# Kernel optimization log

Measured on AMD Instinct MI355X. Metric: run time of the kernel, lower is better.

## Reference

```python
import jax, jax.numpy as jnp
import numpy as np

B, N = 256, 64          # molecules, atoms per molecule
EMB = 64                # atom embedding dim
G = 64                  # n_gaussians
HID = 128               # interaction hidden
OUT = 512               # output_dim
GAUSS_WIDTH = 0.5


def setup_inputs() -> dict:
    key = jax.random.key(0)
    ks = jax.random.split(key, 10)
    atomic_nums = jax.random.randint(ks[0], (B, N), 0, 120, dtype=jnp.int64 if jax.config.x64_enabled else jnp.int32)
    coords = jax.random.normal(ks[1], (B, N, 3), dtype=jnp.float32) * 3.0
    embed_table = jax.random.normal(ks[2], (120, EMB), dtype=jnp.float32)
    # interaction: Linear(128->128), GELU, Linear(128->128); weights stored (in, out)
    W1 = jax.random.normal(ks[3], (EMB + G, HID), dtype=jnp.float32) / np.sqrt(EMB + G)
    b1 = jnp.zeros((HID,), dtype=jnp.float32)
    W2 = jax.random.normal(ks[4], (HID, HID), dtype=jnp.float32) / np.sqrt(HID)
    b2 = jnp.zeros((HID,), dtype=jnp.float32)
    # output_proj: Linear(128 -> 512)
    Wo = jax.random.normal(ks[5], (HID, OUT), dtype=jnp.float32) / np.sqrt(HID)
    bo = jnp.zeros((OUT,), dtype=jnp.float32)
    centers = jnp.linspace(0.0, 10.0, G).astype(jnp.float32)
    return {"atomic_nums": atomic_nums, "coords": coords, "embed_table": embed_table,
            "W1": W1, "b1": b1, "W2": W2, "b2": b2, "Wo": Wo, "bo": bo, "centers": centers}


def reference(atomic_nums, coords, embed_table, W1, b1, W2, b2, Wo, bo, centers):
    # per-atom embedding: [B,N,EMB]
    emb = embed_table[atomic_nums]
    # pairwise distances: [B,N,N]; guard sqrt(0) for diagonal
    diff = coords[:, :, None, :] - coords[:, None, :, :]
    sq = jnp.sum(diff * diff, axis=-1)
    pos = sq > 0
    dists = jnp.where(pos, jnp.sqrt(jnp.where(pos, sq, 1.0)), 0.0)
    # Gaussian smearing: [B,N,N,G]
    gauss = jnp.exp(-0.5 * jnp.square((dists[..., None] - centers) / GAUSS_WIDTH))
    # mean over neighbor axis j: [B,N,G]
    avg_gauss = gauss.mean(axis=2)
    feat = jnp.concatenate([emb, avg_gauss], axis=-1)  # [B,N,EMB+G]
    h = jax.nn.gelu(feat @ W1 + b1, approximate=False) @ W2 + b2  # [B,N,HID]
    mol = h.mean(axis=1)  # [B,HID]
    return mol @ Wo + bo  # [B,OUT]
```

## Files before the change

### kernel.cpp

```cpp
#include <hip/hip_runtime.h>
#include <math.h>

namespace {
constexpr int NB   = 256;
constexpr int NA   = 64;
constexpr int EMBD = 64;
constexpr int HIDD = 128;
constexpr int OUTD = 512;
constexpr int FPS  = 136;
constexpr int DSTR = 68;

typedef __attribute__((ext_vector_type(8))) short bfrag8;
typedef __attribute__((ext_vector_type(4))) float floatx4;

__device__ __forceinline__ unsigned short bf16_rne(float f) {
    unsigned u = __float_as_uint(f);
    u += 0x7fffu + ((u >> 16) & 1u);
    return (unsigned short)(u >> 16);
}

__device__ __forceinline__ float gelu_fast(float x) {
    const float ax = fabsf(x) * 0.7071067811865475f;
    const float t  = __builtin_amdgcn_rcpf(fmaf(0.3275911f, ax, 1.0f));
    float p = fmaf(1.061405429f, t, -1.453152027f);
    p = fmaf(p, t, 1.421413741f);
    p = fmaf(p, t, -0.284496736f);
    p = fmaf(p, t, 0.254829592f);
    p = p * t;
    const float e = __builtin_amdgcn_exp2f(-1.4426950408889634f * ax * ax);
    const float erfx = copysignf(fmaf(-p, e, 1.0f), x);
    const float hx   = 0.5f * x;
    return fmaf(hx, erfx, hx);
}


__global__ __launch_bounds__(1024, 1)
void mlip_fused(const int*   __restrict__ atomic_nums,
                const float* __restrict__ coords,
                const float* __restrict__ embed_table,
                const float* __restrict__ W1, const float* __restrict__ b1,
                const float* __restrict__ W2, const float* __restrict__ b2,
                const float* __restrict__ Wo, const float* __restrict__ bo,
                const float* __restrict__ centers,
                float*       __restrict__ out)
{
    const int b    = blockIdx.x;
    const int tid  = threadIdx.x;
    const int lane = tid & 63;
    const int wid  = tid >> 6;

    __shared__ float s_dist[NA * DSTR];
    __shared__ short s_w[16384];
    __shared__ short s_fhi[NA][FPS];
    __shared__ float s_molS[HIDD];
    __shared__ float s_molv[HIDD];

    const int wn      = wid >> 2;
    const int lrow    = lane & 15, g4 = lane >> 4;
    const int arow    = ((wid & 3) << 4) + lrow;
    const int colbase = (wn << 5) + lrow;

    const int gcol = tid & 127, kc = tid >> 7;
    const int colT = tid >> 1, kh = tid & 1;

    const int grow = tid >> 4;
    const int gch  = (tid >> 2) & 3;
    const int jq   = tid & 3;

    const float bo_r = bo[colT];
    const float b1a  = b1[colbase];
    const float b1b  = b1[colbase + 16];
    const float b2r  = b2[gcol];
    const float c0   = centers[gch << 4];

    if (tid < HIDD) s_molS[tid] = 0.0f;

    float w1v[16];
#pragma unroll
    for (int a = 0; a < 2; ++a) {
        const int slot = (a << 10) + tid;
        const int fg = slot >> 6, ls = slot & 63;
        const int k0 = ((fg >> 3) << 5) + ((ls >> 4) << 3);
        const int n  = ((fg & 7) << 4) + (ls & 15);
        const float* src = W1 + (size_t)k0 * HIDD + n;
#pragma unroll
        for (int r = 0; r < 8; ++r) w1v[a * 8 + r] = src[(size_t)r * HIDD];
    }

    const float* cbase = coords + (size_t)b * NA * 3;
    const float cx = cbase[lane * 3 + 0];
    const float cy = cbase[lane * 3 + 1];
    const float cz = cbase[lane * 3 + 2];
    {
        const int i = tid >> 4, e4 = (tid & 15) << 2;
        const int z = atomic_nums[b * NA + i];
        const float4 ev = *(const float4*)(embed_table + (size_t)z * EMBD + e4);
        short4 h4;
        const float v[4] = {ev.x, ev.y, ev.z, ev.w};
        short* hp = (short*)&h4;
#pragma unroll
        for (int q = 0; q < 4; ++q) hp[q] = (short)bf16_rne(v[q]);
        *(short4*)&s_fhi[i][e4] = h4;
    }

#pragma unroll
    for (int it = 0; it < 4; ++it) {
        const int i = (wid << 2) + it;
        const float xi = __shfl(cx, i, 64);
        const float yi = __shfl(cy, i, 64);
        const float zi = __shfl(cz, i, 64);
        const float dx = xi - cx, dy = yi - cy, dz = zi - cz;
        const float sq = dx * dx + dy * dy + dz * dz;
        s_dist[i * DSTR + lane] = sq > 0.0f ? sqrtf(sq) : 0.0f;
    }

#pragma unroll
    for (int a = 0; a < 2; ++a) {
        unsigned Hu[4];
#pragma unroll
        for (int p = 0; p < 4; ++p) {
            const float x = w1v[a * 8 + 2 * p], y = w1v[a * 8 + 2 * p + 1];
            unsigned h;
            asm("v_cvt_pk_bf16_f32 %0, %1, %2" : "=v"(h) : "v"(x), "v"(y));
            Hu[p] = h;
        }
        const int slot = (a << 10) + tid;
        const int base = ((slot >> 6) << 9) + (slot & 63) * 8;
        *(uint4*)&s_w[base] = make_uint4(Hu[0], Hu[1], Hu[2], Hu[3]);
    }

    {
        constexpr float L2E   = 1.4426950408889634f;
        constexpr float DELTA = 10.0f / 63.0f;
        constexpr float K2L   = -2.0f * L2E;
        constexpr float UA    = 4.0f * DELTA * L2E;
        const float P1  = 0.95085835f,  P2  = 0.81745274f, P3  = 0.63539088f,
                    P4  = 0.44653019f,  P5  = 0.28372112f, P6  = 0.16299117f,
                    P7  = 0.08465801f,  P8  = 0.03975530f, P9  = 0.01688004f,
                    P10 = 0.00647989f,  P11 = 0.00224901f, P12 = 0.00070576f,
                    P13 = 0.00020024f,  P14 = 5.136543e-5f, P15 = 1.191313e-5f;

        float acc[16];
#pragma unroll
        for (int q = 0; q < 16; ++q) acc[q] = 0.0f;

        const float* drow = &s_dist[grow * DSTR + (jq << 4)];
#pragma unroll
        for (int j4 = 0; j4 < 4; ++j4) {
            const float4 d4 = *(const float4*)(drow + (j4 << 2));
            const float dv[4] = {d4.x, d4.y, d4.z, d4.w};
#pragma unroll
            for (int jj = 0; jj < 4; ++jj) {
                const float x  = dv[jj] - c0;
                const float A  = __builtin_amdgcn_exp2f(K2L * x * x);
                const float r  = __builtin_amdgcn_exp2f(UA * x);
                const float r2 = r * r, r4 = r2 * r2;
                float s0 = A, s1 = A * r, s2 = A * r2, s3 = s1 * r2;
                acc[0] += s0;
                acc[1]  = fmaf(s1, P1,  acc[1]);
                acc[2]  = fmaf(s2, P2,  acc[2]);
                acc[3]  = fmaf(s3, P3,  acc[3]);
                s0 *= r4; s1 *= r4; s2 *= r4; s3 *= r4;
                acc[4]  = fmaf(s0, P4,  acc[4]);
                acc[5]  = fmaf(s1, P5,  acc[5]);
                acc[6]  = fmaf(s2, P6,  acc[6]);
                acc[7]  = fmaf(s3, P7,  acc[7]);
                s0 *= r4; s1 *= r4; s2 *= r4; s3 *= r4;
                acc[8]  = fmaf(s0, P8,  acc[8]);
                acc[9]  = fmaf(s1, P9,  acc[9]);
                acc[10] = fmaf(s2, P10, acc[10]);
                acc[11] = fmaf(s3, P11, acc[11]);
                s0 *= r4; s1 *= r4; s2 *= r4; s3 *= r4;
                acc[12] = fmaf(s0, P12, acc[12]);
                acc[13] = fmaf(s1, P13, acc[13]);
                acc[14] = fmaf(s2, P14, acc[14]);
                acc[15] = fmaf(s3, P15, acc[15]);
            }
        }
#pragma unroll
        for (int q = 0; q < 16; ++q) {
            acc[q] += __shfl_xor(acc[q], 1, 64);
            acc[q] += __shfl_xor(acc[q], 2, 64);
        }
        if (jq == 0) {
            unsigned* hp = (unsigned*)&s_fhi[grow][EMBD + (gch << 4)];
#pragma unroll
            for (int q2 = 0; q2 < 8; ++q2) {
                const unsigned h0 = bf16_rne(acc[2 * q2]     * (1.0f / 64.0f));
                const unsigned h1 = bf16_rne(acc[2 * q2 + 1] * (1.0f / 64.0f));
                hp[q2] = h0 | (h1 << 16);
            }
        }
    }
    __syncthreads();

    float wo_a[32];
    float w2r[16];
    {
        floatx4 acc0 = {0,0,0,0}, acc1 = {0,0,0,0};
#pragma unroll
        for (int ks = 0; ks < 4; ++ks) {
            const int k0 = (ks << 5) + (g4 << 3);
            const bfrag8 ahi = *(const bfrag8*)&s_fhi[arow][k0];
#pragma unroll
            for (int nt = 0; nt < 2; ++nt) {
                const int base = ((((ks << 3) + (wn << 1) + nt) << 6) + lane) << 3;
                const bfrag8 bhi = *(const bfrag8*)&s_w[base];
                if (nt) acc1 = __builtin_amdgcn_mfma_f32_16x16x32_bf16(ahi, bhi, acc1, 0, 0, 0);
                else    acc0 = __builtin_amdgcn_mfma_f32_16x16x32_bf16(ahi, bhi, acc0, 0, 0, 0);
            }
        }

        {
            const float* wop = Wo + ((size_t)(kh << 6)) * OUTD + colT;
#pragma unroll
            for (int k = 0; k < 32; ++k) wo_a[k] = wop[(size_t)k * OUTD];
            const float* src = W2 + (size_t)(kc << 4) * HIDD + gcol;
#pragma unroll
            for (int q = 0; q < 16; ++q) w2r[q] = src[(size_t)q * HIDD];
        }

#pragma unroll
        for (int nt = 0; nt < 2; ++nt) {
            const float bb = nt ? b1b : b1a;
            const floatx4 a = nt ? acc1 : acc0;
            float s = gelu_fast(a[0] + bb) + gelu_fast(a[1] + bb)
                    + gelu_fast(a[2] + bb) + gelu_fast(a[3] + bb);
            s += __shfl_xor(s, 16, 64);
            s += __shfl_xor(s, 32, 64);
            if (lane < 16) atomicAdd(&s_molS[colbase + (nt << 4)], s);
        }
    }
    __syncthreads();

    float wo_b[32];
    {
        float acc = 0.0f;
        const int kb = kc << 4;
        float4 m4[4];
#pragma unroll
        for (int p = 0; p < 4; ++p) m4[p] = *(const float4*)&s_molS[kb + (p << 2)];
        const float* ms = (const float*)m4;
#pragma unroll
        for (int q = 0; q < 16; ++q) acc = fmaf(ms[q], w2r[q], acc);
        s_dist[(kc << 7) + gcol] = acc;

        const float* wop = Wo + ((size_t)((kh << 6) + 32)) * OUTD + colT;
#pragma unroll
        for (int k = 0; k < 32; ++k) wo_b[k] = wop[(size_t)k * OUTD];
    }
    __syncthreads();

    if (tid < HIDD) {
        float m = 0.0f;
#pragma unroll
        for (int p = 0; p < 8; ++p) m += s_dist[(p << 7) + tid];
        s_molv[tid] = m * (1.0f / 64.0f) + b2r;
    }
    __syncthreads();

    {
        const float* mp = &s_molv[kh << 6];
        float a = 0.0f;
#pragma unroll
        for (int k = 0; k < 32; ++k) a = fmaf(mp[k], wo_a[k], a);
#pragma unroll
        for (int k = 0; k < 32; ++k) a = fmaf(mp[32 + k], wo_b[k], a);
        a += __shfl_xor(a, 1, 64);
        if (kh == 0)
            out[(size_t)b * OUTD + colT] = a + bo_r;
    }
}
}

extern "C" void kernel_launch(void* const* d_in, const int* in_sizes, int n_in,
                              void* d_out, int out_size, void* d_ws, size_t ws_size,
                              hipStream_t stream) {
    const int*   atomic_nums = (const int*)  d_in[0];
    const float* coords      = (const float*)d_in[1];
    const float* embed_table = (const float*)d_in[2];
    const float* W1          = (const float*)d_in[3];
    const float* b1          = (const float*)d_in[4];
    const float* W2          = (const float*)d_in[5];
    const float* b2          = (const float*)d_in[6];
    const float* Wo          = (const float*)d_in[7];
    const float* bo          = (const float*)d_in[8];
    const float* centers     = (const float*)d_in[9];
    float*       out         = (float*)d_out;

    mlip_fused<<<NB, 1024, 0, stream>>>(atomic_nums, coords, embed_table,
                                        W1, b1, W2, b2, Wo, bo, centers, out);
}
```

Measured before the change: 21.65 us.

## Split fused kernel into per-half-molecule front kernel and separate output projection tail

The single 1024-thread-per-molecule kernel becomes two kernels. The front kernel uses 512 threads per half molecule (512 blocks) to compute features, the W1 MFMA, GELU and the W2 reduction, then writes partial per-molecule vectors to workspace. A second tail kernel sums the two halves, adds b2 and applies the Wo projection. The aim is better occupancy, with fewer registers and less LDS per block and no Wo preloading in registers. The cost is a second launch, a workspace round trip, and each block still staging the full W1 into LDS.

```diff
diff --git a/kernel.cpp b/kernel.cpp
--- a/kernel.cpp
+++ b/kernel.cpp
@@ -33,52 +33,47 @@
     return fmaf(hx, erfx, hx);
 }
 
-
-__global__ __launch_bounds__(1024, 1)
-void mlip_fused(const int*   __restrict__ atomic_nums,
+__global__ __launch_bounds__(512, 4)
+void mlip_front(const int*   __restrict__ atomic_nums,
                 const float* __restrict__ coords,
                 const float* __restrict__ embed_table,
                 const float* __restrict__ W1, const float* __restrict__ b1,
-                const float* __restrict__ W2, const float* __restrict__ b2,
-                const float* __restrict__ Wo, const float* __restrict__ bo,
+                const float* __restrict__ W2,
                 const float* __restrict__ centers,
-                float*       __restrict__ out)
+                float*       __restrict__ ws)
 {
-    const int b    = blockIdx.x;
+    const int bid  = blockIdx.x;
+    const int mol  = bid >> 1, h = bid & 1;
     const int tid  = threadIdx.x;
     const int lane = tid & 63;
     const int wid  = tid >> 6;
 
-    __shared__ float s_dist[NA * DSTR];
+    __shared__ float s_dist[32 * DSTR];
     __shared__ short s_w[16384];
-    __shared__ short s_fhi[NA][FPS];
+    __shared__ short s_fhi[32][FPS];
     __shared__ float s_molS[HIDD];
-    __shared__ float s_molv[HIDD];
-
-    const int wn      = wid >> 2;
+
+    const int wn      = wid >> 1;
     const int lrow    = lane & 15, g4 = lane >> 4;
-    const int arow    = ((wid & 3) << 4) + lrow;
+    const int arow    = ((wid & 1) << 4) + lrow;
     const int colbase = (wn << 5) + lrow;
 
     const int gcol = tid & 127, kc = tid >> 7;
-    const int colT = tid >> 1, kh = tid & 1;
 
     const int grow = tid >> 4;
     const int gch  = (tid >> 2) & 3;
     const int jq   = tid & 3;
 
-    const float bo_r = bo[colT];
-    const float b1a  = b1[colbase];
-    const float b1b  = b1[colbase + 16];
-    const float b2r  = b2[gcol];
-    const float c0   = centers[gch << 4];
+    const float b1a = b1[colbase];
+    const float b1b = b1[colbase + 16];
+    const float c0  = centers[gch << 4];
 
     if (tid < HIDD) s_molS[tid] = 0.0f;
 
     float w1v[16];
 #pragma unroll
     for (int a = 0; a < 2; ++a) {
-        const int slot = (a << 10) + tid;
+        const int slot = (a << 9) + tid;
         const int fg = slot >> 6, ls = slot & 63;
         const int k0 = ((fg >> 3) << 5) + ((ls >> 4) << 3);
         const int n  = ((fg & 7) << 4) + (ls & 15);
@@ -87,13 +82,14 @@
         for (int r = 0; r < 8; ++r) w1v[a * 8 + r] = src[(size_t)r * HIDD];
     }
 
-    const float* cbase = coords + (size_t)b * NA * 3;
+    const float* cbase = coords + (size_t)mol * NA * 3;
     const float cx = cbase[lane * 3 + 0];
     const float cy = cbase[lane * 3 + 1];
     const float cz = cbase[lane * 3 + 2];
+
     {
         const int i = tid >> 4, e4 = (tid & 15) << 2;
-        const int z = atomic_nums[b * NA + i];
+        const int z = atomic_nums[mol * NA + (h << 5) + i];
         const float4 ev = *(const float4*)(embed_table + (size_t)z * EMBD + e4);
         short4 h4;
         const float v[4] = {ev.x, ev.y, ev.z, ev.w};
@@ -105,10 +101,11 @@
 
 #pragma unroll
     for (int it = 0; it < 4; ++it) {
-        const int i = (wid << 2) + it;
-        const float xi = __shfl(cx, i, 64);
-        const float yi = __shfl(cy, i, 64);
-        const float zi = __shfl(cz, i, 64);
+        const int i  = (wid << 2) + it;
+        const int gi = (h << 5) + i;
+        const float xi = __shfl(cx, gi, 64);
+        const float yi = __shfl(cy, gi, 64);
+        const float zi = __shfl(cz, gi, 64);
         const float dx = xi - cx, dy = yi - cy, dz = zi - cz;
         const float sq = dx * dx + dy * dy + dz * dz;
         s_dist[i * DSTR + lane] = sq > 0.0f ? sqrtf(sq) : 0.0f;
@@ -120,13 +117,24 @@
 #pragma unroll
         for (int p = 0; p < 4; ++p) {
             const float x = w1v[a * 8 + 2 * p], y = w1v[a * 8 + 2 * p + 1];
-            unsigned h;
-            asm("v_cvt_pk_bf16_f32 %0, %1, %2" : "=v"(h) : "v"(x), "v"(y));
-            Hu[p] = h;
-        }
-        const int slot = (a << 10) + tid;
+            unsigned hh;
+            asm("v_cvt_pk_bf16_f32 %0, %1, %2" : "=v"(hh) : "v"(x), "v"(y));
+            Hu[p] = hh;
+        }
+        const int slot = (a << 9) + tid;
         const int base = ((slot >> 6) << 9) + (slot & 63) * 8;
         *(uint4*)&s_w[base] = make_uint4(Hu[0], Hu[1], Hu[2], Hu[3]);
+    }
+
+#pragma unroll
+    for (int a = 0; a < 2; ++a) {
+        const int slot = ((a + 2) << 9) + tid;
+        const int fg = slot >> 6, ls = slot & 63;
+        const int k0 = ((fg >> 3) << 5) + ((ls >> 4) << 3);
+        const int n  = ((fg & 7) << 4) + (ls & 15);
+        const float* src = W1 + (size_t)k0 * HIDD + n;
+#pragma unroll
+        for (int r = 0; r < 8; ++r) w1v[a * 8 + r] = src[(size_t)r * HIDD];
     }
 
     {
@@ -192,10 +200,24 @@
             }
         }
     }
+
+#pragma unroll
+    for (int a = 0; a < 2; ++a) {
+        unsigned Hu[4];
+#pragma unroll
+        for (int p = 0; p < 4; ++p) {
+            const float x = w1v[a * 8 + 2 * p], y = w1v[a * 8 + 2 * p + 1];
+            unsigned hh;
+            asm("v_cvt_pk_bf16_f32 %0, %1, %2" : "=v"(hh) : "v"(x), "v"(y));
+            Hu[p] = hh;
+        }
+        const int slot = ((a + 2) << 9) + tid;
+        const int base = ((slot >> 6) << 9) + (slot & 63) * 8;
+        *(uint4*)&s_w[base] = make_uint4(Hu[0], Hu[1], Hu[2], Hu[3]);
+    }
     __syncthreads();
 
-    float wo_a[32];
-    float w2r[16];
+    float w2ra[16];
     {
         floatx4 acc0 = {0,0,0,0}, acc1 = {0,0,0,0};
 #pragma unroll
@@ -212,12 +234,9 @@
         }
 
         {
-            const float* wop = Wo + ((size_t)(kh << 6)) * OUTD + colT;
-#pragma unroll
-            for (int k = 0; k < 32; ++k) wo_a[k] = wop[(size_t)k * OUTD];
-            const float* src = W2 + (size_t)(kc << 4) * HIDD + gcol;
-#pragma unroll
-            for (int q = 0; q < 16; ++q) w2r[q] = src[(size_t)q * HIDD];
+            const float* src = W2 + (size_t)(kc << 5) * HIDD + gcol;
+#pragma unroll
+            for (int q = 0; q < 16; ++q) w2ra[q] = src[(size_t)q * HIDD];
         }
 
 #pragma unroll
@@ -233,43 +252,57 @@
     }
     __syncthreads();
 
-    float wo_b[32];
     {
+        float w2rb[16];
+        const float* src2 = W2 + (size_t)((kc << 5) + 16) * HIDD + gcol;
+#pragma unroll
+        for (int q = 0; q < 16; ++q) w2rb[q] = src2[(size_t)q * HIDD];
+
         float acc = 0.0f;
-        const int kb = kc << 4;
         float4 m4[4];
 #pragma unroll
-        for (int p = 0; p < 4; ++p) m4[p] = *(const float4*)&s_molS[kb + (p << 2)];
+        for (int p = 0; p < 4; ++p) m4[p] = *(const float4*)&s_molS[(kc << 5) + (p << 2)];
         const float* ms = (const float*)m4;
 #pragma unroll
-        for (int q = 0; q < 16; ++q) acc = fmaf(ms[q], w2r[q], acc);
+        for (int q = 0; q < 16; ++q) acc = fmaf(ms[q], w2ra[q], acc);
+        float4 m4b[4];
+#pragma unroll
+        for (int p = 0; p < 4; ++p) m4b[p] = *(const float4*)&s_molS[(kc << 5) + 16 + (p << 2)];
+        const float* ms2 = (const float*)m4b;
+#pragma unroll
+        for (int q = 0; q < 16; ++q) acc = fmaf(ms2[q], w2rb[q], acc);
+
         s_dist[(kc << 7) + gcol] = acc;
-
-        const float* wop = Wo + ((size_t)((kh << 6) + 32)) * OUTD + colT;
-#pragma unroll
-        for (int k = 0; k < 32; ++k) wo_b[k] = wop[(size_t)k * OUTD];
     }
     __syncthreads();
 
     if (tid < HIDD) {
-        float m = 0.0f;
-#pragma unroll
-        for (int p = 0; p < 8; ++p) m += s_dist[(p << 7) + tid];
-        s_molv[tid] = m * (1.0f / 64.0f) + b2r;
-    }
+        const float u = ((s_dist[tid] + s_dist[128 + tid])
+                       + (s_dist[256 + tid] + s_dist[384 + tid])) * (1.0f / 64.0f);
+        ws[(size_t)mol * 256 + (h << 7) + tid] = u;
+    }
+}
+
+__global__ __launch_bounds__(512, 2)
+void mlip_tail(const float* __restrict__ b2,
+               const float* __restrict__ Wo, const float* __restrict__ bo,
+               const float* __restrict__ ws, float* __restrict__ out)
+{
+    const int mol = blockIdx.x;
+    const int tid = threadIdx.x;
+    __shared__ float s_molv[HIDD];
+
+    if (tid < HIDD)
+        s_molv[tid] = (ws[(size_t)mol * 256 + tid] + ws[(size_t)mol * 256 + 128 + tid])
+                      + b2[tid];
     __syncthreads();
 
-    {
-        const float* mp = &s_molv[kh << 6];
-        float a = 0.0f;
-#pragma unroll
-        for (int k = 0; k < 32; ++k) a = fmaf(mp[k], wo_a[k], a);
-#pragma unroll
-        for (int k = 0; k < 32; ++k) a = fmaf(mp[32 + k], wo_b[k], a);
-        a += __shfl_xor(a, 1, 64);
-        if (kh == 0)
-            out[(size_t)b * OUTD + colT] = a + bo_r;
-    }
+    float a = bo[tid];
+    const float* wop = Wo + tid;
+#pragma unroll 8
+    for (int k = 0; k < HIDD; ++k)
+        a = fmaf(s_molv[k], wop[(size_t)k << 9], a);
+    out[(size_t)mol * OUTD + tid] = a;
 }
 }
 
@@ -287,7 +320,9 @@
     const float* bo          = (const float*)d_in[8];
     const float* centers     = (const float*)d_in[9];
     float*       out         = (float*)d_out;
-
-    mlip_fused<<<NB, 1024, 0, stream>>>(atomic_nums, coords, embed_table,
-                                        W1, b1, W2, b2, Wo, bo, centers, out);
-}
+    float*       wsf         = (float*)d_ws;
+
+    mlip_front<<<2 * NB, 512, 0, stream>>>(atomic_nums, coords, embed_table,
+                                           W1, b1, W2, centers, wsf);
+    mlip_tail<<<NB, 512, 0, stream>>>(b2, Wo, bo, wsf, out);
+}
```

Measured after the change: 19.37 us. 10.5% less time.
